# Kernel optimization log

Hardware: AMD Instinct MI355X
Metric: run time of the kernel (lower is better)

The kernel has to match this reference:

```python
import jax, jax.numpy as jnp
import numpy as np
import math

IN_CH = 512
OUT_CH = 512
KSIZE = 3
W_DIM = 512
CONV_SCALE = 1.0 / math.sqrt(IN_CH * KSIZE * KSIZE)
MOD_SCALE = 1.0 / math.sqrt(W_DIM)


def setup_inputs() -> dict:
    key = jax.random.key(0)
    k1, k2, k3, k4 = jax.random.split(key, 4)
    B, H, W = 16, 64, 64
    return {
        "input": jax.random.normal(k1, (B, IN_CH, H, W), dtype=jnp.float32),
        "style": jax.random.normal(k2, (B, W_DIM), dtype=jnp.float32),
        "weight": jax.random.normal(k3, (1, OUT_CH, IN_CH, KSIZE, KSIZE), dtype=jnp.float32),
        "mod_weight": jax.random.normal(k4, (IN_CH, W_DIM), dtype=jnp.float32),
        "mod_bias": jnp.ones((IN_CH,), dtype=jnp.float32),
    }


def reference(input, style, weight, mod_weight, mod_bias):
    B, Cin, H, Wd = input.shape
    # EqualLinear modulation: style -> per-sample, per-input-channel scale
    s = style @ (mod_weight * MOD_SCALE).T + mod_bias  # [B, Cin]
    s = s[:, None, :, None, None]                      # [B,1,Cin,1,1]
    w = CONV_SCALE * weight * s                        # [B,Cout,Cin,k,k]
    demod = jax.lax.rsqrt(jnp.sum(w * w, axis=(2, 3, 4)) + 1e-8)  # [B,Cout]
    w = w * demod[:, :, None, None, None]
    # Grouped conv with groups=batch, same as torch F.conv2d
    w = w.reshape(B * OUT_CH, Cin, KSIZE, KSIZE)
    x = input.reshape(1, B * Cin, H, Wd)
    pad = KSIZE // 2
    out = jax.lax.conv_general_dilated(
        x, w,
        window_strides=(1, 1),
        padding=[(pad, pad), (pad, pad)],
        dimension_numbers=("NCHW", "OIHW", "NCHW"),
        feature_group_count=B,
    )
    return out.reshape(B, OUT_CH, out.shape[2], out.shape[3])
```

## Files before the change

### kernel.cpp

```cpp
#include <hip/hip_runtime.h>
#include <hip/hip_bf16.h>


constexpr float CONV_SCALE = 0.014731391274719738f;
constexpr float MOD_SCALE  = 0.04419417382415922f;

typedef short  bf16x8 __attribute__((ext_vector_type(8)));
typedef float  f32x4  __attribute__((ext_vector_type(4)));

__device__ __forceinline__ unsigned short f2bf(float f) {
  unsigned u = __float_as_uint(f);
  u += 0x7fffu + ((u >> 16) & 1u);
  return (unsigned short)(u >> 16);
}

__device__ __forceinline__ void async16(const void* g, void* l) {
  __builtin_amdgcn_global_load_lds((const __attribute__((address_space(1))) unsigned int*)g,
                                   (__attribute__((address_space(3))) unsigned int*)l,
                                   16, 0, 0);
}

__global__ void k_style(const float* __restrict__ style, const float* __restrict__ mw,
                        const float* __restrict__ mb, float* __restrict__ s) {
  int t = blockIdx.x * 256 + threadIdx.x;
  int b = t & 15, i = t >> 4;
  const float4* st = (const float4*)(style + b * 512);
  const float4* wr = (const float4*)(mw + i * 512);
  float acc = 0.f;
#pragma unroll 8
  for (int j = 0; j < 128; ++j) {
    float4 a = st[j], w4 = wr[j];
    acc += a.x * w4.x + a.y * w4.y + a.z * w4.z + a.w * w4.w;
  }
  s[b * 512 + i] = acc * MOD_SCALE + mb[i];
}

__global__ void k_prepw(const float* __restrict__ w, float* __restrict__ wsq,
                        unsigned short* __restrict__ wt) {
  __shared__ float Wl[2304];
  int t = threadIdx.x;
  size_t base = (size_t)blockIdx.x * 2304;
#pragma unroll
  for (int k = 0; k < 3; ++k) {
    int idx = t + k * 256;
    if (idx < 576) ((float4*)Wl)[idx] = ((const float4*)(w + base))[idx];
  }
  __syncthreads();
  int g = blockIdx.x * 256 + t;
  int ic = g & 511, o = g >> 9;
  float ssq = 0.f;
#pragma unroll
  for (int tap = 0; tap < 9; ++tap) {
    float v = Wl[t * 9 + tap];
    ssq += v * v;
    wt[((size_t)tap * 512 + o) * 512 + ic] = f2bf(v);
  }
  wsq[o * 512 + ic] = ssq;
}

__global__ void k_dscale(const float* __restrict__ s, const float* __restrict__ wsq,
                         float* __restrict__ dscale) {
  int t = blockIdx.x * 256 + threadIdx.x;
  int b = t & 15, o = t >> 4;
  const float4* sq = (const float4*)(wsq + o * 512);
  const float4* sb = (const float4*)(s + b * 512);
  float acc = 0.f;
#pragma unroll 8
  for (int j = 0; j < 128; ++j) {
    float4 q4 = sq[j], s4 = sb[j];
    acc += q4.x * s4.x * s4.x + q4.y * s4.y * s4.y + q4.z * s4.z * s4.z + q4.w * s4.w * s4.w;
  }
  float d = rsqrtf(CONV_SCALE * CONV_SCALE * acc + 1e-8f);
  dscale[b * 512 + o] = d * CONV_SCALE;
}

__global__ void k_xt(const float* __restrict__ x, const float* __restrict__ s,
                     unsigned short* __restrict__ xt) {
  __shared__ float T[64][68];
  int h = blockIdx.x, b = blockIdx.y;
  const float* xp = x + (size_t)b * 512 * 4096 + h * 64;
  unsigned short* xo = xt + ((size_t)(b * 64 + h) * 64) * 512;
  int t = threadIdx.x;
  for (int ic0 = 0; ic0 < 512; ic0 += 64) {
#pragma unroll
    for (int k = 0; k < 4; ++k) {
      int idx = t + k * 256;
      int icl = idx >> 4, c4 = idx & 15;
      int ic = ic0 + icl;
      float4 v = *(const float4*)&xp[(size_t)ic * 4096 + c4 * 4];
      float sc = s[b * 512 + ic];
      v.x *= sc; v.y *= sc; v.z *= sc; v.w *= sc;
      *(float4*)&T[icl][c4 * 4] = v;
    }
    __syncthreads();
#pragma unroll
    for (int c = t; c < 512; c += 256) {
      int wv = c >> 3, ig = (c & 7) * 8;
      unsigned p0 = (unsigned)f2bf(T[ig + 0][wv]) | ((unsigned)f2bf(T[ig + 1][wv]) << 16);
      unsigned p1 = (unsigned)f2bf(T[ig + 2][wv]) | ((unsigned)f2bf(T[ig + 3][wv]) << 16);
      unsigned p2 = (unsigned)f2bf(T[ig + 4][wv]) | ((unsigned)f2bf(T[ig + 5][wv]) << 16);
      unsigned p3 = (unsigned)f2bf(T[ig + 6][wv]) | ((unsigned)f2bf(T[ig + 7][wv]) << 16);
      uint4 pk = {p0, p1, p2, p3};
      *(uint4*)&xo[(size_t)wv * 512 + ic0 + ig] = pk;
    }
    __syncthreads();
  }
}

__global__ __launch_bounds__(256, 2)
void k_conv(const unsigned short* __restrict__ xt, const unsigned short* __restrict__ wt,
            const float* __restrict__ dscale, float* __restrict__ out) {
  __shared__ short Xs[6 * 66 * 32];
  __shared__ short Ws[3 * 128 * 32];

  const int b  = blockIdx.z;
  const int o0 = blockIdx.y * 128;
  const int h0 = blockIdx.x * 4;
  const int t = threadIdx.x;
  const int wave = t >> 6, lane = t & 63;
  const int q = lane >> 4, l16 = lane & 15;

  f32x4 acc[8][4];
#pragma unroll
  for (int i = 0; i < 8; ++i)
#pragma unroll
    for (int j = 0; j < 4; ++j) acc[i][j] = (f32x4){0.f, 0.f, 0.f, 0.f};

  if (t < 192) {
    int r = t >> 5, rem = t & 31;
    int col = (rem >> 4) * 65, ch2 = (rem & 15) * 2;
    *(int*)&Xs[(r * 66 + col) * 32 + ch2] = 0;
  }

  int xrowi[6]; bool xval[6];
#pragma unroll
  for (int j = 0; j < 6; ++j) {
    int c = wave * 6 + j;
    int row = c >> 2;
    int hg = h0 - 1 + row;
    xval[j] = (hg >= 0) && (hg < 64);
    xrowi[j] = c;
    (void)xrowi;
  }

  for (int ic0 = 0; ic0 < 512; ic0 += 32) {
    __syncthreads();
#pragma unroll
    for (int j = 0; j < 6; ++j) {
      int c = wave * 6 + j;
      int row = c >> 2, q16 = c & 3;
      int hg = h0 - 1 + row;
      short* dst = &Xs[(row * 66 + 1 + q16 * 16) * 32];
      if (xval[j]) {
        const unsigned short* src =
            xt + ((size_t)((b * 64 + hg) * 64) + q16 * 16 + (lane >> 2)) * 512 + ic0 + (lane & 3) * 8;
        async16(src, dst);
      } else {
        *(int4*)&dst[lane * 8] = (int4){0, 0, 0, 0};
      }
    }
#pragma unroll
    for (int kh = 0; kh < 3; ++kh) {
      if (kh) __syncthreads();
#pragma unroll
      for (int j = 0; j < 6; ++j) {
        int ci = wave * 6 + j;
        int kw = ci >> 3, oo = ((ci & 7) << 4) + (lane >> 2);
        async16(wt + (((size_t)(kh * 3 + kw) * 512 + o0 + oo) * 512 + ic0 + (lane & 3) * 8),
                &Ws[ci * 512]);
      }
      __syncthreads();
      const short* xbase = &Xs[(wave + kh) * 66 * 32 + q * 8];
#pragma unroll
      for (int kw = 0; kw < 3; ++kw) {
        bf16x8 bfr[4];
#pragma unroll
        for (int ni = 0; ni < 4; ++ni)
          bfr[ni] = *(const bf16x8*)&xbase[(ni * 16 + l16 + kw) * 32];
#pragma unroll
        for (int mi = 0; mi < 8; ++mi) {
          bf16x8 af = *(const bf16x8*)&Ws[(kw * 128 + mi * 16 + l16) * 32 + q * 8];
#pragma unroll
          for (int ni = 0; ni < 4; ++ni)
            acc[mi][ni] = __builtin_amdgcn_mfma_f32_16x16x32_bf16(af, bfr[ni], acc[mi][ni], 0, 0, 0);
        }
      }
    }
  }

  const int h = h0 + wave;
#pragma unroll
  for (int mi = 0; mi < 8; ++mi) {
#pragma unroll
    for (int r = 0; r < 4; ++r) {
      int o_l = mi * 16 + q * 4 + r;
      float ds = dscale[b * 512 + o0 + o_l];
      float* orow = out + ((size_t)(b * 512 + o0 + o_l) * 64 + h) * 64;
#pragma unroll
      for (int ni = 0; ni < 4; ++ni)
        orow[ni * 16 + l16] = acc[mi][ni][r] * ds;
    }
  }
}

extern "C" void kernel_launch(void* const* d_in, const int* in_sizes, int n_in,
                              void* d_out, int out_size, void* d_ws, size_t ws_size,
                              hipStream_t stream) {
  const float* x      = (const float*)d_in[0];
  const float* style  = (const float*)d_in[1];
  const float* weight = (const float*)d_in[2];
  const float* mw     = (const float*)d_in[3];
  const float* mb     = (const float*)d_in[4];
  float* out = (float*)d_out;

  float* s      = (float*)d_ws;
  float* dscale = s + 8192;
  float* wsq    = dscale + 8192;
  unsigned short* wt = (unsigned short*)(wsq + 262144);
  unsigned short* xt = wt + 9 * 512 * 512;

  k_style<<<32, 256, 0, stream>>>(style, mw, mb, s);
  k_prepw<<<1024, 256, 0, stream>>>(weight, wsq, wt);
  k_dscale<<<32, 256, 0, stream>>>(s, wsq, dscale);
  k_xt<<<dim3(64, 16), 256, 0, stream>>>(x, s, xt);
  k_conv<<<dim3(16, 4, 16), 256, 0, stream>>>(xt, wt, dscale, out);
}
```

Measured before the change: 516.8 us.

## Double-buffer conv staging, pad input rows in memory, swizzle LDS layouts

```diff
diff --git a/kernel.cpp b/kernel.cpp
--- a/kernel.cpp
+++ b/kernel.cpp
@@ -74,12 +74,21 @@
   dscale[b * 512 + o] = d * CONV_SCALE;
 }
 
+__global__ void k_zpad(unsigned short* __restrict__ xt) {
+  int strip = blockIdx.x;
+  int b = strip >> 1, sel = strip & 1;
+  unsigned short* p = xt + ((size_t)(b * 66 + sel * 65) * 64) * 512;
+  int4 z = {0, 0, 0, 0};
+  for (int idx = threadIdx.x; idx < 4096; idx += 256)
+    ((int4*)p)[idx] = z;
+}
+
 __global__ void k_xt(const float* __restrict__ x, const float* __restrict__ s,
                      unsigned short* __restrict__ xt) {
   __shared__ float T[64][68];
   int h = blockIdx.x, b = blockIdx.y;
   const float* xp = x + (size_t)b * 512 * 4096 + h * 64;
-  unsigned short* xo = xt + ((size_t)(b * 64 + h) * 64) * 512;
+  unsigned short* xo = xt + ((size_t)((b * 66) + h + 1) * 64) * 512;
   int t = threadIdx.x;
   for (int ic0 = 0; ic0 < 512; ic0 += 64) {
 #pragma unroll
@@ -90,16 +99,17 @@
       float4 v = *(const float4*)&xp[(size_t)ic * 4096 + c4 * 4];
       float sc = s[b * 512 + ic];
       v.x *= sc; v.y *= sc; v.z *= sc; v.w *= sc;
-      *(float4*)&T[icl][c4 * 4] = v;
+      *(float4*)&T[icl][(c4 ^ (icl >> 3)) << 2] = v;
     }
     __syncthreads();
 #pragma unroll
     for (int c = t; c < 512; c += 256) {
       int wv = c >> 3, ig = (c & 7) * 8;
-      unsigned p0 = (unsigned)f2bf(T[ig + 0][wv]) | ((unsigned)f2bf(T[ig + 1][wv]) << 16);
-      unsigned p1 = (unsigned)f2bf(T[ig + 2][wv]) | ((unsigned)f2bf(T[ig + 3][wv]) << 16);
-      unsigned p2 = (unsigned)f2bf(T[ig + 4][wv]) | ((unsigned)f2bf(T[ig + 5][wv]) << 16);
-      unsigned p3 = (unsigned)f2bf(T[ig + 6][wv]) | ((unsigned)f2bf(T[ig + 7][wv]) << 16);
+      int colf = ((((c >> 3) >> 2) ^ (c & 7)) << 2) + ((c >> 3) & 3);
+      unsigned p0 = (unsigned)f2bf(T[ig + 0][colf]) | ((unsigned)f2bf(T[ig + 1][colf]) << 16);
+      unsigned p1 = (unsigned)f2bf(T[ig + 2][colf]) | ((unsigned)f2bf(T[ig + 3][colf]) << 16);
+      unsigned p2 = (unsigned)f2bf(T[ig + 4][colf]) | ((unsigned)f2bf(T[ig + 5][colf]) << 16);
+      unsigned p3 = (unsigned)f2bf(T[ig + 6][colf]) | ((unsigned)f2bf(T[ig + 7][colf]) << 16);
       uint4 pk = {p0, p1, p2, p3};
       *(uint4*)&xo[(size_t)wv * 512 + ic0 + ig] = pk;
     }
@@ -107,86 +117,112 @@
   }
 }
 
-__global__ __launch_bounds__(256, 2)
+__global__ __launch_bounds__(512, 2)
 void k_conv(const unsigned short* __restrict__ xt, const unsigned short* __restrict__ wt,
             const float* __restrict__ dscale, float* __restrict__ out) {
-  __shared__ short Xs[6 * 66 * 32];
-  __shared__ short Ws[3 * 128 * 32];
+  __shared__ short Xs[2][10 * 66 * 32];
+  __shared__ short Ws[2][3 * 128 * 32];
 
   const int b  = blockIdx.z;
   const int o0 = blockIdx.y * 128;
-  const int h0 = blockIdx.x * 4;
+  const int h0 = blockIdx.x * 8;
   const int t = threadIdx.x;
   const int wave = t >> 6, lane = t & 63;
   const int q = lane >> 4, l16 = lane & 15;
 
+  const int xsrc8 = ((lane & 3) ^ ((((lane >> 2) + 1) >> 1) & 3)) * 8;
+  const int wsrc8 = ((lane & 3) ^ ((lane >> 3) & 3)) * 8;
+  const int wq8 = (q ^ ((l16 >> 1) & 3)) * 8;
+
   f32x4 acc[8][4];
 #pragma unroll
   for (int i = 0; i < 8; ++i)
 #pragma unroll
     for (int j = 0; j < 4; ++j) acc[i][j] = (f32x4){0.f, 0.f, 0.f, 0.f};
 
-  if (t < 192) {
-    int r = t >> 5, rem = t & 31;
+  for (int z = t; z < 640; z += 512) {
+    int bi = (z >= 320) ? 1 : 0;
+    int zz = z - bi * 320;
+    int r = zz >> 5, rem = zz & 31;
     int col = (rem >> 4) * 65, ch2 = (rem & 15) * 2;
-    *(int*)&Xs[(r * 66 + col) * 32 + ch2] = 0;
-  }
-
-  int xrowi[6]; bool xval[6];
-#pragma unroll
-  for (int j = 0; j < 6; ++j) {
-    int c = wave * 6 + j;
-    int row = c >> 2;
-    int hg = h0 - 1 + row;
-    xval[j] = (hg >= 0) && (hg < 64);
-    xrowi[j] = c;
-    (void)xrowi;
-  }
-
-  for (int ic0 = 0; ic0 < 512; ic0 += 32) {
-    __syncthreads();
-#pragma unroll
-    for (int j = 0; j < 6; ++j) {
-      int c = wave * 6 + j;
+    *(int*)&Xs[bi][(r * 66 + col) * 32 + ch2] = 0;
+  }
+
+  auto stageX = [&](int i_, int xb_) {
+    int ic0_ = i_ * 32;
+#pragma unroll
+    for (int j = 0; j < 5; ++j) {
+      int c = wave * 5 + j;
       int row = c >> 2, q16 = c & 3;
-      int hg = h0 - 1 + row;
-      short* dst = &Xs[(row * 66 + 1 + q16 * 16) * 32];
-      if (xval[j]) {
-        const unsigned short* src =
-            xt + ((size_t)((b * 64 + hg) * 64) + q16 * 16 + (lane >> 2)) * 512 + ic0 + (lane & 3) * 8;
-        async16(src, dst);
-      } else {
-        *(int4*)&dst[lane * 8] = (int4){0, 0, 0, 0};
+      async16(xt + ((size_t)((b * 66 + h0 + row) * 64) + q16 * 16 + (lane >> 2)) * 512 + ic0_ + xsrc8,
+              &Xs[xb_][(row * 66 + 1 + q16 * 16) * 32]);
+    }
+  };
+  auto stageW = [&](int i_, int kh_, int wb_) {
+    int ic0_ = i_ * 32;
+#pragma unroll
+    for (int j = 0; j < 3; ++j) {
+      int ci = wave * 3 + j;
+      int kw = ci >> 3, oo = ((ci & 7) << 4) + (lane >> 2);
+      async16(wt + (((size_t)(kh_ * 3 + kw) * 512 + o0 + oo) * 512 + ic0_ + wsrc8),
+              &Ws[wb_][ci * 512]);
+    }
+  };
+  auto compute = [&](int kh, int xb_, int wb_) {
+    const short* Xrow = &Xs[xb_][(wave + kh) * 66 * 32];
+    const short* Wb = Ws[wb_];
+    __builtin_amdgcn_s_setprio(1);
+#pragma unroll
+    for (int kw = 0; kw < 3; ++kw) {
+      bf16x8 bfr[4];
+#pragma unroll
+      for (int ni = 0; ni < 4; ++ni) {
+        int c = ni * 16 + l16 + kw;
+        bfr[ni] = *(const bf16x8*)&Xrow[c * 32 + ((q ^ ((c >> 1) & 3)) << 3)];
       }
-    }
-#pragma unroll
-    for (int kh = 0; kh < 3; ++kh) {
-      if (kh) __syncthreads();
-#pragma unroll
-      for (int j = 0; j < 6; ++j) {
-        int ci = wave * 6 + j;
-        int kw = ci >> 3, oo = ((ci & 7) << 4) + (lane >> 2);
-        async16(wt + (((size_t)(kh * 3 + kw) * 512 + o0 + oo) * 512 + ic0 + (lane & 3) * 8),
-                &Ws[ci * 512]);
+#pragma unroll
+      for (int mi = 0; mi < 8; ++mi) {
+        bf16x8 af = *(const bf16x8*)&Wb[(kw * 128 + mi * 16 + l16) * 32 + wq8];
+#pragma unroll
+        for (int ni = 0; ni < 4; ++ni)
+          acc[mi][ni] = __builtin_amdgcn_mfma_f32_16x16x32_bf16(af, bfr[ni], acc[mi][ni], 0, 0, 0);
       }
-      __syncthreads();
-      const short* xbase = &Xs[(wave + kh) * 66 * 32 + q * 8];
-#pragma unroll
-      for (int kw = 0; kw < 3; ++kw) {
-        bf16x8 bfr[4];
-#pragma unroll
-        for (int ni = 0; ni < 4; ++ni)
-          bfr[ni] = *(const bf16x8*)&xbase[(ni * 16 + l16 + kw) * 32];
-#pragma unroll
-        for (int mi = 0; mi < 8; ++mi) {
-          bf16x8 af = *(const bf16x8*)&Ws[(kw * 128 + mi * 16 + l16) * 32 + q * 8];
-#pragma unroll
-          for (int ni = 0; ni < 4; ++ni)
-            acc[mi][ni] = __builtin_amdgcn_mfma_f32_16x16x32_bf16(af, bfr[ni], acc[mi][ni], 0, 0, 0);
-        }
-      }
-    }
-  }
+    }
+    __builtin_amdgcn_s_setprio(0);
+  };
+
+  stageX(0, 0);
+  stageW(0, 0, 0);
+  __syncthreads();
+
+#pragma unroll 2
+  for (int i = 0; i < 16; ++i) {
+    const int xb = i & 1;
+    const int inext = (i < 15) ? i + 1 : 15;
+    stageW(i, 1, xb ^ 1);
+    stageX(inext, xb ^ 1);
+    asm volatile("s_waitcnt vmcnt(8)" ::: "memory");
+    __builtin_amdgcn_s_barrier();
+    __builtin_amdgcn_sched_barrier(0);
+    compute(0, xb, xb);
+    __builtin_amdgcn_sched_barrier(0);
+    __builtin_amdgcn_s_barrier();
+    stageW(i, 2, xb);
+    asm volatile("s_waitcnt vmcnt(8)" ::: "memory");
+    __builtin_amdgcn_s_barrier();
+    __builtin_amdgcn_sched_barrier(0);
+    compute(1, xb, xb ^ 1);
+    __builtin_amdgcn_sched_barrier(0);
+    __builtin_amdgcn_s_barrier();
+    stageW(inext, 0, xb ^ 1);
+    asm volatile("s_waitcnt vmcnt(3)" ::: "memory");
+    __builtin_amdgcn_s_barrier();
+    __builtin_amdgcn_sched_barrier(0);
+    compute(2, xb, xb);
+    __builtin_amdgcn_sched_barrier(0);
+    __builtin_amdgcn_s_barrier();
+  }
+  asm volatile("s_waitcnt vmcnt(0)" ::: "memory");
 
   const int h = h0 + wave;
 #pragma unroll
@@ -222,6 +258,7 @@
   k_style<<<32, 256, 0, stream>>>(style, mw, mb, s);
   k_prepw<<<1024, 256, 0, stream>>>(weight, wsq, wt);
   k_dscale<<<32, 256, 0, stream>>>(s, wsq, dscale);
+  k_zpad<<<32, 256, 0, stream>>>(xt);
   k_xt<<<dim3(64, 16), 256, 0, stream>>>(x, s, xt);
-  k_conv<<<dim3(16, 4, 16), 256, 0, stream>>>(xt, wt, dscale, out);
-}
+  k_conv<<<dim3(8, 4, 16), 512, 0, stream>>>(xt, wt, dscale, out);
+}
```

New measurement: 526.7 us. Within noise of the previous version (+1.9%).
